# Kernel tuning notes

Hardware: AMD Instinct MI355X
Metric: run time of the kernel (lower is better)

Reference implementation:

```python
import jax, jax.numpy as jnp
import numpy as np

HID = 768
INNER = 1536   # hidden_size * expand_factor
NSTATE = 16
KCONV = 4
EPS = 1e-5


def _layernorm(x, w, b):
    mu = jnp.mean(x, axis=-1, keepdims=True)
    var = jnp.mean(jnp.square(x - mu), axis=-1, keepdims=True)
    return (x - mu) * jax.lax.rsqrt(var + EPS) * w + b


def setup_inputs() -> dict:
    key = jax.random.key(0)
    ks = jax.random.split(key, 8)
    B, S = 2, 2048
    s_in = 1.0 / np.sqrt(HID).astype(np.float32)
    s_inner = 1.0 / np.sqrt(INNER).astype(np.float32)
    s_k = 1.0 / np.sqrt(KCONV).astype(np.float32)
    return {
        "x": jax.random.normal(ks[0], (B, S, HID), jnp.float32),
        "norm_w": jnp.ones((HID,), jnp.float32),
        "norm_b": jnp.zeros((HID,), jnp.float32),
        "W_in": jax.random.normal(ks[1], (HID, 2 * INNER), jnp.float32) * s_in,
        "conv_w": jax.random.normal(ks[2], (INNER, 1, KCONV), jnp.float32) * s_k,  # OIH depthwise
        "W_xproj": jax.random.normal(ks[3], (INNER, 2 * NSTATE + INNER), jnp.float32) * s_inner,
        "A_log": jax.random.normal(ks[4], (NSTATE,), jnp.float32),
        "D": jnp.ones((INNER,), jnp.float32),
        "W_ssm_out": jax.random.normal(ks[5], (INNER, INNER), jnp.float32) * s_inner,
        "W_out": jax.random.normal(ks[6], (INNER, HID), jnp.float32) * s_inner,
    }


def _selective_ssm(u, W_xproj, A_log, D, W_ssm_out):
    # u: (B, S, INNER)
    proj = u @ W_xproj                                   # (B,S,2N+INNER)
    Bm = proj[..., :NSTATE]                              # (B,S,N)
    Cm = proj[..., NSTATE:2 * NSTATE]                    # (B,S,N)
    delta = jax.nn.softplus(proj[..., 2 * NSTATE:])      # (B,S,INNER)
    A = -jnp.exp(A_log)                                  # (N,)

    def step(h, inp):
        d_t, b_t, c_t, u_t = inp                          # (B,INNER),(B,N),(B,N),(B,INNER)
        dA = jnp.exp(d_t[:, None, :] * A[None, :, None])  # (B,N,INNER)
        h = dA * h + (d_t * u_t)[:, None, :] * b_t[:, :, None]
        y = jnp.einsum('bnh,bn->bh', h, c_t)
        return h, y

    B_, S_, _ = u.shape
    h0 = jnp.zeros((B_, NSTATE, INNER), u.dtype)
    xs = (jnp.moveaxis(delta, 1, 0), jnp.moveaxis(Bm, 1, 0),
          jnp.moveaxis(Cm, 1, 0), jnp.moveaxis(u, 1, 0))
    _, ys = jax.lax.scan(step, h0, xs)                   # (S,B,INNER)
    y = jnp.moveaxis(ys, 0, 1) + D * u
    return y @ W_ssm_out


def reference(x, norm_w, norm_b, W_in, conv_w, W_xproj, A_log, D, W_ssm_out, W_out):
    residual = x
    xn = _layernorm(x, norm_w, norm_b)
    xp = xn @ W_in                                       # (B,S,2*INNER)
    u, gate = jnp.split(xp, 2, axis=-1)
    # causal depthwise conv1d (torch pads k-1 both sides then truncates -> left pad k-1)
    uc = jax.lax.conv_general_dilated(
        jnp.swapaxes(u, 1, 2), conv_w, window_strides=(1,),
        padding=[(KCONV - 1, 0)], dimension_numbers=('NCH', 'OIH', 'NCH'),
        feature_group_count=INNER)
    u = jax.nn.silu(jnp.swapaxes(uc, 1, 2))              # (B,S,INNER)
    y = _selective_ssm(u, W_xproj, A_log, D, W_ssm_out)
    y = y * jax.nn.silu(gate)
    out = y @ W_out + residual                           # dropout is identity in eval
    return out
```

## Files before the change

kernel.cpp:

```cpp
#include <hip/hip_runtime.h>
#include <cstdint>
#include <cmath>

#define HID 768
#define INNER 1536
#define NST 16
#define SEQ 2048
#define BATCH 2
#define MTOK 4096
#define CHUNK 32
#define NCHUNK 64
#define LOG2E 1.44269504088896f

typedef unsigned short u16;
typedef __bf16 bf16x8 __attribute__((ext_vector_type(8)));
typedef float f32x4 __attribute__((ext_vector_type(4)));

__device__ __forceinline__ u16 f2b(float f) {
  union { float f; unsigned u; } a; a.f = f;
  unsigned r = a.u + 0x7FFFu + ((a.u >> 16) & 1u);
  return (u16)(r >> 16);
}

__device__ __forceinline__ void gl2lds16(const u16* g, u16* l) {
  __builtin_amdgcn_global_load_lds(
      (const __attribute__((address_space(1))) void*)g,
      (__attribute__((address_space(3))) void*)l, 16, 0, 0);
}

__global__ __launch_bounds__(256)
void ln_kernel(const float* __restrict__ x, const float* __restrict__ w,
               const float* __restrict__ b, u16* __restrict__ xn) {
  const long row = blockIdx.x;
  const float* xr = x + row * HID;
  const int t = threadIdx.x;
  float v0 = xr[t], v1 = xr[t + 256], v2 = xr[t + 512];
  float s1 = v0 + v1 + v2;
  float s2 = v0 * v0 + v1 * v1 + v2 * v2;
#pragma unroll
  for (int o = 32; o > 0; o >>= 1) { s1 += __shfl_down(s1, o); s2 += __shfl_down(s2, o); }
  __shared__ float r1[4], r2[4];
  if ((t & 63) == 0) { r1[t >> 6] = s1; r2[t >> 6] = s2; }
  __syncthreads();
  s1 = r1[0] + r1[1] + r1[2] + r1[3];
  s2 = r2[0] + r2[1] + r2[2] + r2[3];
  const float mu = s1 * (1.f / HID);
  float var = s2 * (1.f / HID) - mu * mu;
  const float rs = rsqrtf(var + 1e-5f);
  xn[row * HID + t]       = f2b((v0 - mu) * rs * w[t]       + b[t]);
  xn[row * HID + t + 256] = f2b((v1 - mu) * rs * w[t + 256] + b[t + 256]);
  xn[row * HID + t + 512] = f2b((v2 - mu) * rs * w[t + 512] + b[t + 512]);
}

__global__ __launch_bounds__(256)
void transpose_cvt(const float* __restrict__ W, u16* __restrict__ Wt,
                   int K, int N, int Npad) {
  __shared__ float tb[32][33];
  const int tx = threadIdx.x, ty = threadIdx.y;
  const int n0 = blockIdx.x * 32, k0 = blockIdx.y * 32;
#pragma unroll
  for (int r = 0; r < 4; ++r) {
    int kk = k0 + ty + r * 8;
    int nn = n0 + tx;
    tb[ty + r * 8][tx] = (nn < N) ? W[(long)kk * N + nn] : 0.f;
  }
  __syncthreads();
#pragma unroll
  for (int r = 0; r < 4; ++r) {
    int nn = n0 + ty + r * 8;
    int kk = k0 + tx;
    Wt[(long)nn * K + kk] = f2b(tb[tx][ty + r * 8]);
  }
}

template <int BM, int BN, int EPI>
__global__ __launch_bounds__(256)
void gemm_bt(const u16* __restrict__ A, const u16* __restrict__ Bt,
             float* __restrict__ C0, float* __restrict__ C1, float* __restrict__ C2,
             u16* __restrict__ Cb, const float* __restrict__ E0,
             int K, int Nstore) {
  constexpr int WTM = BM / 2;
  constexpr int WTN = BN / 2;
  constexpr int FI = WTM / 16;
  constexpr int FJ = WTN / 16;
  __shared__ u16 As[BM * 32];
  __shared__ u16 Bs[BN * 32];
  const int tid = threadIdx.x;
  const int lane = tid & 63;
  const int wave = tid >> 6;
  const int wm = wave >> 1, wn = wave & 1;
  const int l16 = lane & 15, l4 = lane >> 4;
  const long bm = (long)blockIdx.y * BM;
  const long bn = (long)blockIdx.x * BN;

  f32x4 acc[FI][FJ] = {};

  const int r0 = tid >> 2;
  const int kg = (tid & 3) * 8;

  for (int k0 = 0; k0 < K; k0 += 32) {
#pragma unroll
    for (int q = 0; q < BM / 64; ++q)
      gl2lds16(A + (bm + r0 + q * 64) * K + kg + k0, As + ((q * 256 + tid) * 8));
#pragma unroll
    for (int q = 0; q < BN / 64; ++q)
      gl2lds16(Bt + (bn + r0 + q * 64) * K + kg + k0, Bs + ((q * 256 + tid) * 8));
    __syncthreads();
    bf16x8 af[FI], bfr[FJ];
#pragma unroll
    for (int i = 0; i < FI; ++i)
      af[i] = *(const bf16x8*)&As[(wm * WTM + i * 16 + l16) * 32 + l4 * 8];
#pragma unroll
    for (int j = 0; j < FJ; ++j)
      bfr[j] = *(const bf16x8*)&Bs[(wn * WTN + j * 16 + l16) * 32 + l4 * 8];
#pragma unroll
    for (int i = 0; i < FI; ++i)
#pragma unroll
      for (int j = 0; j < FJ; ++j)
        acc[i][j] = __builtin_amdgcn_mfma_f32_16x16x32_bf16(af[i], bfr[j], acc[i][j], 0, 0, 0);
    __syncthreads();
  }

#pragma unroll
  for (int i = 0; i < FI; ++i) {
    const long rr = bm + wm * WTM + i * 16 + l4 * 4;
#pragma unroll
    for (int j = 0; j < FJ; ++j) {
      const int cc = (int)bn + wn * WTN + j * 16 + l16;
#pragma unroll
      for (int r = 0; r < 4; ++r) {
        const long row = rr + r;
        const float v = acc[i][j][r];
        if (EPI == 0) {
          C0[row * 3072 + cc] = v;
        } else if (EPI == 1) {
          if (cc < 16) C0[row * 16 + cc] = v;
          else if (cc < 32) C1[row * 16 + (cc - 16)] = v;
          else if (cc < Nstore) {
            float sp = (v > 20.f) ? v : log1pf(__expf(v));
            C2[row * 1536 + (cc - 32)] = sp;
          }
        } else if (EPI == 2) {
          float g = E0[row * 3072 + 1536 + cc];
          float s = g / (1.f + __expf(-g));
          Cb[row * 1536 + cc] = f2b(v * s);
        } else {
          C0[row * 768 + cc] = v + E0[row * 768 + cc];
        }
      }
    }
  }
}

__global__ __launch_bounds__(256)
void conv_silu(const float* __restrict__ xp, const float* __restrict__ cw,
               float* __restrict__ uf, u16* __restrict__ ub) {
  const int c = blockIdx.x * 256 + threadIdx.x;
  const long m = blockIdx.y;
  const int t = (int)(m & (SEQ - 1));
  const float w0 = cw[c * 4 + 0], w1 = cw[c * 4 + 1], w2 = cw[c * 4 + 2], w3 = cw[c * 4 + 3];
  float acc = w3 * xp[m * 3072 + c];
  if (t >= 1) acc += w2 * xp[(m - 1) * 3072 + c];
  if (t >= 2) acc += w1 * xp[(m - 2) * 3072 + c];
  if (t >= 3) acc += w0 * xp[(m - 3) * 3072 + c];
  const float s = acc / (1.f + __expf(-acc));
  uf[m * 1536 + c] = s;
  ub[m * 1536 + c] = f2b(s);
}

__global__ __launch_bounds__(256)
void scan_phaseA(const float* __restrict__ dlt, const float* __restrict__ uf,
                 const float* __restrict__ Bm, const float* __restrict__ A_log,
                 float* __restrict__ P, float* __restrict__ Q) {
  const int tid = threadIdx.x;
  const int cl = tid >> 2;
  const int sg = tid & 3;
  const int c = blockIdx.x * 64 + cl;
  const int b = blockIdx.y;
  const int ch = blockIdx.z;
  float a2[4];
#pragma unroll
  for (int j = 0; j < 4; ++j) a2[j] = -__expf(A_log[sg * 4 + j]) * LOG2E;
  float h[4] = {0.f, 0.f, 0.f, 0.f};
  float sumd = 0.f;
  const long base = (long)b * SEQ + (long)ch * CHUNK;
  for (int t = 0; t < CHUNK; ++t) {
    const long m = base + t;
    const float d = dlt[m * 1536 + c];
    const float du = d * uf[m * 1536 + c];
    sumd += d;
    const f32x4 Bv = *(const f32x4*)&Bm[m * 16 + sg * 4];
#pragma unroll
    for (int j = 0; j < 4; ++j) {
      const float e = exp2f(a2[j] * d);
      h[j] = e * h[j] + du * Bv[j];
    }
  }
  const long sb = (((long)b * NCHUNK + ch) * NST + sg * 4) * 1536 + c;
#pragma unroll
  for (int j = 0; j < 4; ++j) {
    Q[sb + (long)j * 1536] = h[j];
    P[sb + (long)j * 1536] = exp2f(a2[j] * sumd);
  }
}

__global__ __launch_bounds__(256)
void scan_phaseB(float* __restrict__ P, const float* __restrict__ Q) {
  const long g = (long)blockIdx.x * 256 + threadIdx.x;
  const int c = (int)(g % 1536);
  const int n = (int)((g / 1536) % NST);
  const int b = (int)(g / (1536 * NST));
  float h = 0.f;
  for (int ch = 0; ch < NCHUNK; ++ch) {
    const long idx = (((long)b * NCHUNK + ch) * NST + n) * 1536 + c;
    const float p = P[idx];
    const float q = Q[idx];
    P[idx] = h;
    h = p * h + q;
  }
}

__global__ __launch_bounds__(256)
void scan_phaseC(const float* __restrict__ dlt, const float* __restrict__ uf,
                 const float* __restrict__ Bm, const float* __restrict__ Cm,
                 const float* __restrict__ A_log, const float* __restrict__ Dv,
                 const float* __restrict__ hs, u16* __restrict__ ys) {
  const int tid = threadIdx.x;
  const int cl = tid >> 2;
  const int sg = tid & 3;
  const int c = blockIdx.x * 64 + cl;
  const int b = blockIdx.y;
  const int ch = blockIdx.z;
  float a2[4];
#pragma unroll
  for (int j = 0; j < 4; ++j) a2[j] = -__expf(A_log[sg * 4 + j]) * LOG2E;
  float h[4];
  const long sb = (((long)b * NCHUNK + ch) * NST + sg * 4) * 1536 + c;
#pragma unroll
  for (int j = 0; j < 4; ++j) h[j] = hs[sb + (long)j * 1536];
  const float Dc = Dv[c];
  const long base = (long)b * SEQ + (long)ch * CHUNK;
  for (int t = 0; t < CHUNK; ++t) {
    const long m = base + t;
    const float d = dlt[m * 1536 + c];
    const float uu = uf[m * 1536 + c];
    const float du = d * uu;
    const f32x4 Bv = *(const f32x4*)&Bm[m * 16 + sg * 4];
    const f32x4 Cv = *(const f32x4*)&Cm[m * 16 + sg * 4];
    float y = (sg == 0) ? Dc * uu : 0.f;
#pragma unroll
    for (int j = 0; j < 4; ++j) {
      const float e = exp2f(a2[j] * d);
      h[j] = e * h[j] + du * Bv[j];
      y += h[j] * Cv[j];
    }
    y += __shfl_xor(y, 1);
    y += __shfl_xor(y, 2);
    if (sg == 0) ys[m * 1536 + c] = f2b(y);
  }
}

extern "C" void kernel_launch(void* const* d_in, const int* in_sizes, int n_in,
                              void* d_out, int out_size, void* d_ws, size_t ws_size,
                              hipStream_t stream) {
  const float* x     = (const float*)d_in[0];
  const float* nw    = (const float*)d_in[1];
  const float* nb    = (const float*)d_in[2];
  const float* W_in  = (const float*)d_in[3];
  const float* cw    = (const float*)d_in[4];
  const float* W_xp  = (const float*)d_in[5];
  const float* A_log = (const float*)d_in[6];
  const float* Dv    = (const float*)d_in[7];
  const float* W_so  = (const float*)d_in[8];
  const float* W_out = (const float*)d_in[9];
  float* out = (float*)d_out;

  char* w = (char*)d_ws;
  auto alloc = [&](size_t bytes) {
    char* p = w;
    w += (bytes + 255) & ~(size_t)255;
    return p;
  };
  u16*   xn    = (u16*)  alloc((size_t)MTOK * HID * 2);
  u16*   WtIn  = (u16*)  alloc((size_t)3072 * 768 * 2);
  float* xp    = (float*)alloc((size_t)MTOK * 3072 * 4);
  float* uf    = (float*)alloc((size_t)MTOK * 1536 * 4);
  u16*   ub    = (u16*)  alloc((size_t)MTOK * 1536 * 2);
  u16*   WtXp  = (u16*)  alloc((size_t)1664 * 1536 * 2);
  float* Bmv   = (float*)alloc((size_t)MTOK * 16 * 4);
  float* Cmv   = (float*)alloc((size_t)MTOK * 16 * 4);
  float* dlt   = (float*)alloc((size_t)MTOK * 1536 * 4);
  float* P     = (float*)alloc((size_t)BATCH * NCHUNK * NST * 1536 * 4);
  float* Q     = (float*)alloc((size_t)BATCH * NCHUNK * NST * 1536 * 4);
  u16*   ys    = (u16*)  alloc((size_t)MTOK * 1536 * 2);
  u16*   WtSo  = (u16*)  alloc((size_t)1536 * 1536 * 2);
  u16*   zb    = (u16*)  alloc((size_t)MTOK * 1536 * 2);
  u16*   WtOut = (u16*)  alloc((size_t)768 * 1536 * 2);

  ln_kernel<<<MTOK, 256, 0, stream>>>(x, nw, nb, xn);
  transpose_cvt<<<dim3(3072 / 32, 768 / 32), dim3(32, 8), 0, stream>>>(W_in, WtIn, 768, 3072, 3072);
  transpose_cvt<<<dim3(1664 / 32, 1536 / 32), dim3(32, 8), 0, stream>>>(W_xp, WtXp, 1536, 1568, 1664);
  transpose_cvt<<<dim3(1536 / 32, 1536 / 32), dim3(32, 8), 0, stream>>>(W_so, WtSo, 1536, 1536, 1536);
  transpose_cvt<<<dim3(768 / 32, 1536 / 32), dim3(32, 8), 0, stream>>>(W_out, WtOut, 1536, 768, 768);

  gemm_bt<128, 128, 0><<<dim3(24, 32), 256, 0, stream>>>(xn, WtIn, xp, nullptr, nullptr, nullptr, nullptr, 768, 3072);
  conv_silu<<<dim3(6, MTOK), 256, 0, stream>>>(xp, cw, uf, ub);
  gemm_bt<128, 64, 1><<<dim3(26, 32), 256, 0, stream>>>(ub, WtXp, Bmv, Cmv, dlt, nullptr, nullptr, 1536, 1568);
  scan_phaseA<<<dim3(24, 2, NCHUNK), 256, 0, stream>>>(dlt, uf, Bmv, A_log, P, Q);
  scan_phaseB<<<192, 256, 0, stream>>>(P, Q);
  scan_phaseC<<<dim3(24, 2, NCHUNK), 256, 0, stream>>>(dlt, uf, Bmv, Cmv, A_log, Dv, P, ys);
  gemm_bt<128, 64, 2><<<dim3(24, 32), 256, 0, stream>>>(ys, WtSo, nullptr, nullptr, nullptr, zb, xp, 1536, 1536);
  gemm_bt<64, 64, 3><<<dim3(12, 64), 256, 0, stream>>>(zb, WtOut, out, nullptr, nullptr, nullptr, x, 1536, 768);
}
```

Measured before the change: 398.6 us.

## Shrink intermediates to bf16, precompute gate silu, remap GEMM blocks per XCD

The input-projection GEMM epilogue now splits its output. It stores u in fp32 and silu(gate) as bf16, so the later GEMM reads a precomputed bf16 gate instead of recomputing silu from fp32. Delta and the conv output are stored and read only as bf16 by the scans, which removes the fp32 uf buffer and halves dlt traffic. GEMM launches become 1D with a block-to-tile mapping that groups contiguous row tiles on each XCD for L2 locality. The cost is reduced precision in the scan inputs (delta and u in bf16).

```diff
diff --git a/kernel.cpp b/kernel.cpp
--- a/kernel.cpp
+++ b/kernel.cpp
@@ -20,6 +20,9 @@
   union { float f; unsigned u; } a; a.f = f;
   unsigned r = a.u + 0x7FFFu + ((a.u >> 16) & 1u);
   return (u16)(r >> 16);
+}
+__device__ __forceinline__ float b2f(u16 h) {
+  union { unsigned u; float f; } a; a.u = ((unsigned)h) << 16; return a.f;
 }
 
 __device__ __forceinline__ void gl2lds16(const u16* g, u16* l) {
@@ -73,25 +76,33 @@
   }
 }
 
-template <int BM, int BN, int EPI>
+template <int BM, int BN, int NBX, int EPI>
 __global__ __launch_bounds__(256)
 void gemm_bt(const u16* __restrict__ A, const u16* __restrict__ Bt,
-             float* __restrict__ C0, float* __restrict__ C1, float* __restrict__ C2,
-             u16* __restrict__ Cb, const float* __restrict__ E0,
+             float* __restrict__ O0, float* __restrict__ O1, u16* __restrict__ O2,
+             const float* __restrict__ Ef, const u16* __restrict__ Eb,
              int K, int Nstore) {
+  constexpr int NBY = 4096 / BM;
+  constexpr int PER = NBY / 8;
   constexpr int WTM = BM / 2;
   constexpr int WTN = BN / 2;
   constexpr int FI = WTM / 16;
   constexpr int FJ = WTN / 16;
   __shared__ u16 As[BM * 32];
   __shared__ u16 Bs[BN * 32];
+  const int u = blockIdx.x;
+  const int xcd = u & 7;
+  const int s = u >> 3;
+  const int bmt = xcd * PER + s / NBX;
+  const int bnt = s % NBX;
+  const long bm = (long)bmt * BM;
+  const long bn = (long)bnt * BN;
+
   const int tid = threadIdx.x;
   const int lane = tid & 63;
   const int wave = tid >> 6;
   const int wm = wave >> 1, wn = wave & 1;
   const int l16 = lane & 15, l4 = lane >> 4;
-  const long bm = (long)blockIdx.y * BM;
-  const long bn = (long)blockIdx.x * BN;
 
   f32x4 acc[FI][FJ] = {};
 
@@ -132,20 +143,23 @@
         const long row = rr + r;
         const float v = acc[i][j][r];
         if (EPI == 0) {
-          C0[row * 3072 + cc] = v;
+          if (cc < 1536) O0[row * 1536 + cc] = v;
+          else {
+            float sv = v / (1.f + __expf(-v));
+            O2[row * 1536 + (cc - 1536)] = f2b(sv);
+          }
         } else if (EPI == 1) {
-          if (cc < 16) C0[row * 16 + cc] = v;
-          else if (cc < 32) C1[row * 16 + (cc - 16)] = v;
+          if (cc < 16) O0[row * 16 + cc] = v;
+          else if (cc < 32) O1[row * 16 + (cc - 16)] = v;
           else if (cc < Nstore) {
             float sp = (v > 20.f) ? v : log1pf(__expf(v));
-            C2[row * 1536 + (cc - 32)] = sp;
+            O2[row * 1536 + (cc - 32)] = f2b(sp);
           }
         } else if (EPI == 2) {
-          float g = E0[row * 3072 + 1536 + cc];
-          float s = g / (1.f + __expf(-g));
-          Cb[row * 1536 + cc] = f2b(v * s);
+          float g = b2f(Eb[row * 1536 + cc]);
+          O2[row * 1536 + cc] = f2b(v * g);
         } else {
-          C0[row * 768 + cc] = v + E0[row * 768 + cc];
+          O0[row * 768 + cc] = v + Ef[row * 768 + cc];
         }
       }
     }
@@ -153,23 +167,22 @@
 }
 
 __global__ __launch_bounds__(256)
-void conv_silu(const float* __restrict__ xp, const float* __restrict__ cw,
-               float* __restrict__ uf, u16* __restrict__ ub) {
+void conv_silu(const float* __restrict__ xpu, const float* __restrict__ cw,
+               u16* __restrict__ ub) {
   const int c = blockIdx.x * 256 + threadIdx.x;
   const long m = blockIdx.y;
   const int t = (int)(m & (SEQ - 1));
   const float w0 = cw[c * 4 + 0], w1 = cw[c * 4 + 1], w2 = cw[c * 4 + 2], w3 = cw[c * 4 + 3];
-  float acc = w3 * xp[m * 3072 + c];
-  if (t >= 1) acc += w2 * xp[(m - 1) * 3072 + c];
-  if (t >= 2) acc += w1 * xp[(m - 2) * 3072 + c];
-  if (t >= 3) acc += w0 * xp[(m - 3) * 3072 + c];
+  float acc = w3 * xpu[m * 1536 + c];
+  if (t >= 1) acc += w2 * xpu[(m - 1) * 1536 + c];
+  if (t >= 2) acc += w1 * xpu[(m - 2) * 1536 + c];
+  if (t >= 3) acc += w0 * xpu[(m - 3) * 1536 + c];
   const float s = acc / (1.f + __expf(-acc));
-  uf[m * 1536 + c] = s;
   ub[m * 1536 + c] = f2b(s);
 }
 
 __global__ __launch_bounds__(256)
-void scan_phaseA(const float* __restrict__ dlt, const float* __restrict__ uf,
+void scan_phaseA(const u16* __restrict__ dlt, const u16* __restrict__ ub,
                  const float* __restrict__ Bm, const float* __restrict__ A_log,
                  float* __restrict__ P, float* __restrict__ Q) {
   const int tid = threadIdx.x;
@@ -186,8 +199,8 @@
   const long base = (long)b * SEQ + (long)ch * CHUNK;
   for (int t = 0; t < CHUNK; ++t) {
     const long m = base + t;
-    const float d = dlt[m * 1536 + c];
-    const float du = d * uf[m * 1536 + c];
+    const float d = b2f(dlt[m * 1536 + c]);
+    const float du = d * b2f(ub[m * 1536 + c]);
     sumd += d;
     const f32x4 Bv = *(const f32x4*)&Bm[m * 16 + sg * 4];
 #pragma unroll
@@ -221,7 +234,7 @@
 }
 
 __global__ __launch_bounds__(256)
-void scan_phaseC(const float* __restrict__ dlt, const float* __restrict__ uf,
+void scan_phaseC(const u16* __restrict__ dlt, const u16* __restrict__ ub,
                  const float* __restrict__ Bm, const float* __restrict__ Cm,
                  const float* __restrict__ A_log, const float* __restrict__ Dv,
                  const float* __restrict__ hs, u16* __restrict__ ys) {
@@ -242,8 +255,8 @@
   const long base = (long)b * SEQ + (long)ch * CHUNK;
   for (int t = 0; t < CHUNK; ++t) {
     const long m = base + t;
-    const float d = dlt[m * 1536 + c];
-    const float uu = uf[m * 1536 + c];
+    const float d = b2f(dlt[m * 1536 + c]);
+    const float uu = b2f(ub[m * 1536 + c]);
     const float du = d * uu;
     const f32x4 Bv = *(const f32x4*)&Bm[m * 16 + sg * 4];
     const f32x4 Cv = *(const f32x4*)&Cm[m * 16 + sg * 4];
@@ -283,13 +296,13 @@
   };
   u16*   xn    = (u16*)  alloc((size_t)MTOK * HID * 2);
   u16*   WtIn  = (u16*)  alloc((size_t)3072 * 768 * 2);
-  float* xp    = (float*)alloc((size_t)MTOK * 3072 * 4);
-  float* uf    = (float*)alloc((size_t)MTOK * 1536 * 4);
+  float* xpu   = (float*)alloc((size_t)MTOK * 1536 * 4);
+  u16*   sg    = (u16*)  alloc((size_t)MTOK * 1536 * 2);
   u16*   ub    = (u16*)  alloc((size_t)MTOK * 1536 * 2);
   u16*   WtXp  = (u16*)  alloc((size_t)1664 * 1536 * 2);
   float* Bmv   = (float*)alloc((size_t)MTOK * 16 * 4);
   float* Cmv   = (float*)alloc((size_t)MTOK * 16 * 4);
-  float* dlt   = (float*)alloc((size_t)MTOK * 1536 * 4);
+  u16*   dlt   = (u16*)  alloc((size_t)MTOK * 1536 * 2);
   float* P     = (float*)alloc((size_t)BATCH * NCHUNK * NST * 1536 * 4);
   float* Q     = (float*)alloc((size_t)BATCH * NCHUNK * NST * 1536 * 4);
   u16*   ys    = (u16*)  alloc((size_t)MTOK * 1536 * 2);
@@ -303,12 +316,12 @@
   transpose_cvt<<<dim3(1536 / 32, 1536 / 32), dim3(32, 8), 0, stream>>>(W_so, WtSo, 1536, 1536, 1536);
   transpose_cvt<<<dim3(768 / 32, 1536 / 32), dim3(32, 8), 0, stream>>>(W_out, WtOut, 1536, 768, 768);
 
-  gemm_bt<128, 128, 0><<<dim3(24, 32), 256, 0, stream>>>(xn, WtIn, xp, nullptr, nullptr, nullptr, nullptr, 768, 3072);
-  conv_silu<<<dim3(6, MTOK), 256, 0, stream>>>(xp, cw, uf, ub);
-  gemm_bt<128, 64, 1><<<dim3(26, 32), 256, 0, stream>>>(ub, WtXp, Bmv, Cmv, dlt, nullptr, nullptr, 1536, 1568);
-  scan_phaseA<<<dim3(24, 2, NCHUNK), 256, 0, stream>>>(dlt, uf, Bmv, A_log, P, Q);
+  gemm_bt<128, 128, 24, 0><<<768, 256, 0, stream>>>(xn, WtIn, xpu, nullptr, sg, nullptr, nullptr, 768, 3072);
+  conv_silu<<<dim3(6, MTOK), 256, 0, stream>>>(xpu, cw, ub);
+  gemm_bt<128, 64, 26, 1><<<832, 256, 0, stream>>>(ub, WtXp, Bmv, Cmv, dlt, nullptr, nullptr, 1536, 1568);
+  scan_phaseA<<<dim3(24, 2, NCHUNK), 256, 0, stream>>>(dlt, ub, Bmv, A_log, P, Q);
   scan_phaseB<<<192, 256, 0, stream>>>(P, Q);
-  scan_phaseC<<<dim3(24, 2, NCHUNK), 256, 0, stream>>>(dlt, uf, Bmv, Cmv, A_log, Dv, P, ys);
-  gemm_bt<128, 64, 2><<<dim3(24, 32), 256, 0, stream>>>(ys, WtSo, nullptr, nullptr, nullptr, zb, xp, 1536, 1536);
-  gemm_bt<64, 64, 3><<<dim3(12, 64), 256, 0, stream>>>(zb, WtOut, out, nullptr, nullptr, nullptr, x, 1536, 768);
-}
+  scan_phaseC<<<dim3(24, 2, NCHUNK), 256, 0, stream>>>(dlt, ub, Bmv, Cmv, A_log, Dv, P, ys);
+  gemm_bt<128, 64, 24, 2><<<768, 256, 0, stream>>>(ys, WtSo, nullptr, nullptr, zb, nullptr, sg, 1536, 1536);
+  gemm_bt<64, 64, 12, 3><<<768, 256, 0, stream>>>(zb, WtOut, out, nullptr, nullptr, x, nullptr, 1536, 768);
+}
```

Result: no change. 399.1 us (+0.1%).
